# Kernel optimization log

Hardware: AMD Instinct MI355X
Metric: run time of the kernel (lower is better)

Reference implementation:

```python
import jax, jax.numpy as jnp
import numpy as np

UNITS = 512
LN_EPS = 1e-3  # Keras LayerNormalization default epsilon


def _lstm_cell(x, h, c, W, U, b):
    # Keras LSTMCell: z = x@W + h@U + b, gate order [i, f, g, o]
    z = x @ W + h @ U + b
    i, f, g, o = jnp.split(z, 4, axis=-1)
    i = jax.nn.sigmoid(i)
    f = jax.nn.sigmoid(f)
    g = jnp.tanh(g)
    o = jax.nn.sigmoid(o)
    c_new = f * c + i * g
    h_new = o * jnp.tanh(c_new)
    return h_new, c_new


def _layernorm(x, gamma, beta):
    mu = jnp.mean(x, axis=-1, keepdims=True)
    var = jnp.mean(jnp.square(x - mu), axis=-1, keepdims=True)
    return (x - mu) * jax.lax.rsqrt(var + LN_EPS) * gamma + beta


def setup_inputs() -> dict:
    key = jax.random.key(0)
    ks = jax.random.split(key, 8)
    B, T, F, U, C = 128, 1000, 72, UNITS, 14
    s = 0.05
    return {
        "x": jax.random.normal(ks[0], (B, T, F), jnp.float32),
        "w0": jax.random.normal(ks[1], (F, 4 * U), jnp.float32) * s,
        "u0": jax.random.normal(ks[2], (U, 4 * U), jnp.float32) * s,
        "b0": jnp.zeros((4 * U,), jnp.float32),
        "gamma": jnp.ones((U,), jnp.float32),
        "beta": jnp.zeros((U,), jnp.float32),
        "w1": jax.random.normal(ks[3], (U, 4 * U), jnp.float32) * s,
        "u1": jax.random.normal(ks[4], (U, 4 * U), jnp.float32) * s,
        "b1": jnp.zeros((4 * U,), jnp.float32),
        "wf": jax.random.normal(ks[5], (U, C), jnp.float32) * s,
        "bf": jnp.zeros((C,), jnp.float32),
    }


def reference(x, w0, u0, b0, gamma, beta, w1, u1, b1, wf, bf):
    B = x.shape[0]
    U = UNITS
    xt = jnp.transpose(x, (1, 0, 2))  # [T, B, F] time-major
    init = (
        jnp.zeros((B, U), x.dtype), jnp.zeros((B, U), x.dtype),  # h0, c0
        jnp.zeros((B, U), x.dtype), jnp.zeros((B, U), x.dtype),  # h1, c1
    )

    def step(carry, x_t):
        h0, c0, h1, c1 = carry
        h0, c0 = _lstm_cell(x_t, h0, c0, w0, u0, b0)
        h0n = _layernorm(h0, gamma, beta)
        h1, c1 = _lstm_cell(h0n, h1, c1, w1, u1, b1)
        # dropout is identity at inference (training=False)
        y_t = jax.nn.softmax(h1 @ wf + bf, axis=-1)
        return (h0, c0, h1, c1), y_t

    _, ys = jax.lax.scan(step, init, xt)  # ys: [T, B, C]
    return jnp.transpose(ys, (1, 0, 2))   # [B, T, C]
```

## Files before the change

kernel.cpp:

```cpp
#include <hip/hip_runtime.h>
#include <cstdint>
#include <cstddef>

#define T_STEPS 1000
#define NU 512
#define NC 14

typedef unsigned short ushort_t;
typedef unsigned int uint_t;
typedef __attribute__((ext_vector_type(8))) short bf16x8;
typedef __attribute__((ext_vector_type(4))) float f32x4;

#define OFF_BP0H  0u
#define OFF_BP0L  (OFF_BP0H + 128u*9728u*2u)
#define OFF_BP1H  (OFF_BP0L + 128u*9728u*2u)
#define OFF_BP1L  (OFF_BP1H + 128u*16384u*2u)
#define OFF_S1P   (OFF_BP1L + 128u*16384u*2u)
#define OFF_ZB1P  (OFF_S1P  + 2048u*4u)
#define OFF_B0P   (OFF_ZB1P + 2048u*4u)
#define OFF_WFT   (OFF_B0P  + 2048u*4u)
#define OFF_H0H   (OFF_WFT  + 14u*512u*4u)
#define OFF_H0L   (OFF_H0H  + 262144u)
#define OFF_H1H   (OFF_H0L  + 262144u)
#define OFF_H1L   (OFF_H1H  + 262144u)
#define OFF_CTR   (OFF_H1L  + 262144u)

#define SLOT_C0SUB  0
#define SLOT_C0ROOT (8*64)
#define SLOT_C1SUB  (16*64)
#define SLOT_C1ROOT (24*64)

__device__ __forceinline__ float bf2f(short s) {
    unsigned u = ((unsigned)(unsigned short)s) << 16;
    return __builtin_bit_cast(float, u);
}
__device__ __forceinline__ ushort_t f2bf(float f) {
    unsigned u = __float_as_uint(f);
    u = u + 0x7FFFu + ((u >> 16) & 1u);
    return (ushort_t)(u >> 16);
}

__global__ void pack0_kernel(const float* __restrict__ w0, const float* __restrict__ u0,
                             ushort_t* __restrict__ bp0h, ushort_t* __restrict__ bp0l)
{
    const int ntile = blockIdx.x;
    const int l = threadIdx.x & 63;
    const int c = l & 15, koff = (l >> 4) * 8;
    const int zcol = ntile * 4 + (c >> 2) + 512 * (c & 3);
    for (int s = (threadIdx.x >> 6); s < 19; s += 4) {
        bf16x8 hv, lv;
#pragma unroll
        for (int j = 0; j < 8; ++j) {
            int k = s * 32 + koff + j;
            float v;
            if (k < 96) v = (k < 72) ? w0[(size_t)k * 2048 + zcol] : 0.f;
            else        v = u0[(size_t)(k - 96) * 2048 + zcol];
            ushort_t hi = f2bf(v);
            ushort_t lo = f2bf(v - bf2f((short)hi));
            hv[j] = (short)hi; lv[j] = (short)lo;
        }
        size_t di = ((size_t)(ntile * 19 + s) * 64 + l) * 8;
        *(bf16x8*)&bp0h[di] = hv;
        *(bf16x8*)&bp0l[di] = lv;
    }
}

__global__ void pack1_kernel(const float* __restrict__ w1, const float* __restrict__ u1,
                             const float* __restrict__ gamma,
                             ushort_t* __restrict__ bp1h, ushort_t* __restrict__ bp1l)
{
    const int ntile = blockIdx.x;
    const int l = threadIdx.x & 63;
    const int c = l & 15, koff = (l >> 4) * 8;
    const int zcol = ntile * 4 + (c >> 2) + 512 * (c & 3);
    for (int s = (threadIdx.x >> 6); s < 32; s += 4) {
        bf16x8 hv, lv;
#pragma unroll
        for (int j = 0; j < 8; ++j) {
            int k = s * 32 + koff + j;
            float v = (k < 512) ? gamma[k] * w1[(size_t)k * 2048 + zcol]
                                : u1[(size_t)(k - 512) * 2048 + zcol];
            ushort_t hi = f2bf(v);
            ushort_t lo = f2bf(v - bf2f((short)hi));
            hv[j] = (short)hi; lv[j] = (short)lo;
        }
        size_t di = ((size_t)(ntile * 32 + s) * 64 + l) * 8;
        *(bf16x8*)&bp1h[di] = hv;
        *(bf16x8*)&bp1l[di] = lv;
    }
}

__global__ void sums_kernel(const float* __restrict__ w1, const float* __restrict__ gamma,
                            const float* __restrict__ beta, const float* __restrict__ b0,
                            const float* __restrict__ b1,
                            float* __restrict__ s1p, float* __restrict__ zb1p,
                            float* __restrict__ b0p)
{
    int zcol = blockIdx.x * 256 + threadIdx.x;
    float gs = 0.f, bs = 0.f;
    for (int k = 0; k < NU; k++) {
        float w = w1[(size_t)k * 2048 + zcol];
        gs += gamma[k] * w;
        bs += beta[k] * w;
    }
    int g = zcol >> 9, r = zcol & 511, nt = r >> 2, u = r & 3;
    int pc = nt * 16 + u * 4 + g;
    s1p[pc]  = gs;
    zb1p[pc] = b1[zcol] + bs;
    b0p[pc]  = b0[zcol];
}

__global__ void wft_kernel(const float* __restrict__ wf, float* __restrict__ wfT)
{
    int i = blockIdx.x * 512 + threadIdx.x;
    if (i < NC * NU) {
        int c = i >> 9, u = i & 511;
        wfT[c * NU + u] = wf[(size_t)u * NC + c];
    }
}

__global__ void init_kernel(char* __restrict__ ws)
{
    size_t i = (size_t)blockIdx.x * 1024 + threadIdx.x;
    uint_t* st = (uint_t*)(ws + OFF_H0H);
    if (i < 262144) st[i] = 0u;
    if (i < 2048) ((uint_t*)(ws + OFF_CTR))[i] = 0u;
}

__device__ __forceinline__ float sigf(float x)     { return 1.f / (1.f + __expf(-x)); }
__device__ __forceinline__ float tanhfast(float x) { return 2.f / (1.f + __expf(-2.f * x)) - 1.f; }

__device__ __forceinline__ void wait_ge(const unsigned* p, unsigned tgt)
{
    while (__hip_atomic_load(p, __ATOMIC_RELAXED, __HIP_MEMORY_SCOPE_AGENT) < tgt)
        __builtin_amdgcn_s_sleep(1);
}

__device__ __forceinline__ void publish(unsigned* sub, unsigned* root)
{
    unsigned old = __hip_atomic_fetch_add(sub, 1u, __ATOMIC_RELAXED, __HIP_MEMORY_SCOPE_AGENT);
    if ((old & 15u) == 15u)
        __hip_atomic_fetch_add(root, 16u, __ATOMIC_RELAXED, __HIP_MEMORY_SCOPE_AGENT);
}

__device__ void ypass(const ushort_t* __restrict__ h1h, const ushort_t* __restrict__ h1l,
                      const float* __restrict__ wfT, const float* __restrict__ bf,
                      float* __restrict__ out, int b, int tw, int lane)
{
    bf16x8 hh = *(const bf16x8*)(h1h + (size_t)b * NU + lane * 8);
    bf16x8 hl = *(const bf16x8*)(h1l + (size_t)b * NU + lane * 8);
    float hv[8];
#pragma unroll
    for (int j = 0; j < 8; ++j) hv[j] = bf2f(hh[j]) + bf2f(hl[j]);
    float z[NC];
#pragma unroll
    for (int c = 0; c < NC; ++c) {
        const float* wp = wfT + c * NU + lane * 8;
        float a = 0.f;
#pragma unroll
        for (int j = 0; j < 8; ++j) a = fmaf(hv[j], wp[j], a);
        z[c] = a;
    }
#pragma unroll
    for (int off = 32; off > 0; off >>= 1) {
#pragma unroll
        for (int c = 0; c < NC; ++c) z[c] += __shfl_xor(z[c], off);
    }
    if (lane == 0) {
        float mx = -1e30f;
#pragma unroll
        for (int c = 0; c < NC; ++c) { z[c] += bf[c]; mx = fmaxf(mx, z[c]); }
        float s = 0.f, e[NC];
#pragma unroll
        for (int c = 0; c < NC; ++c) { e[c] = __expf(z[c] - mx); s += e[c]; }
        float inv = 1.f / s;
        float* o = out + ((size_t)b * T_STEPS + tw) * NC;
#pragma unroll
        for (int c = 0; c < NC; ++c) o[c] = e[c] * inv;
    }
}

#define MFMA(A,B,C) __builtin_amdgcn_mfma_f32_16x16x32_bf16((A),(B),(C),0,0,0)

__global__ __launch_bounds__(512, 1)
void lstm_main(const float* __restrict__ x, const float* __restrict__ bf,
               char* __restrict__ ws, float* __restrict__ out)
{
    __shared__ __attribute__((aligned(16))) unsigned char smem[98304];

    const float* __restrict__ s1p  = (const float*)(ws + OFF_S1P);
    const float* __restrict__ zb1p = (const float*)(ws + OFF_ZB1P);
    const float* __restrict__ b0p  = (const float*)(ws + OFF_B0P);
    const float* __restrict__ wfT  = (const float*)(ws + OFF_WFT);
    ushort_t* h0h = (ushort_t*)(ws + OFF_H0H);
    ushort_t* h0l = (ushort_t*)(ws + OFF_H0L);
    ushort_t* h1h = (ushort_t*)(ws + OFF_H1H);
    ushort_t* h1l = (ushort_t*)(ws + OFF_H1L);
    unsigned* ctr = (unsigned*)(ws + OFF_CTR);

    const int tid  = threadIdx.x;
    const int l    = tid & 63;
    const int w    = tid >> 6;
    const int rr   = l & 15;
    const int koff = (l >> 4) * 8;
    const int blk  = blockIdx.x;
    const int erow = tid >> 2, eu = tid & 3;

    unsigned* C0root = ctr + SLOT_C0ROOT;
    unsigned* C1root = ctr + SLOT_C1ROOT;

    if (blk < 128) {
        const int ntile = blk;
        ushort_t* bpAh = (ushort_t*)smem;
        ushort_t* bpAl = (ushort_t*)(smem + 19456);
        ushort_t* xsh  = (ushort_t*)(smem + 38912);
        ushort_t* xsl  = (ushort_t*)(smem + 63488);
        float*    zex  = (float*)(smem + 88064);
        unsigned* C0sub = ctr + SLOT_C0SUB + (blk & 7) * 64;

        {
            const uint_t* sh = (const uint_t*)(ws + OFF_BP0H) + (size_t)ntile * 4864;
            const uint_t* sl = (const uint_t*)(ws + OFF_BP0L) + (size_t)ntile * 4864;
            uint_t* dh = (uint_t*)bpAh; uint_t* dl = (uint_t*)bpAl;
            for (int i = tid; i < 4864; i += 512) { dh[i] = sh[i]; dl[i] = sl[i]; }
            uint_t* xz = (uint_t*)xsh;
            for (int i = tid; i < 12288; i += 512) xz[i] = 0u;
        }
        const f32x4 b0v = *(const f32x4*)&b0p[ntile * 16 + eu * 4];
        float c0v = 0.f;
        const int m = w;
        const int rowA = m * 16 + rr;
        __syncthreads();

#pragma unroll 1
        for (int t = 0; t < T_STEPS; ++t) {
            const int cur = t & 1, prv = cur ^ 1;
            ushort_t* __restrict__       h0h_cur = h0h + cur * 65536;
            ushort_t* __restrict__       h0l_cur = h0l + cur * 65536;
            const ushort_t* __restrict__ h0h_prv = h0h + prv * 65536;
            const ushort_t* __restrict__ h0l_prv = h0l + prv * 65536;

#pragma unroll
            for (int i = 0; i < 18; ++i) {
                int e = tid + i * 512;
                int row = e / 72, k = e - row * 72;
                float v = x[(size_t)row * 72000 + (size_t)t * 72 + k];
                ushort_t hi = f2bf(v);
                ushort_t lo = f2bf(v - bf2f((short)hi));
                int di = (((row >> 4) * 3 + (k >> 5)) * 64 + ((k >> 3) & 3) * 16 + (row & 15)) * 8 + (k & 7);
                xsh[di] = hi; xsl[di] = lo;
            }
            if (tid == 0) {
                if (t >= 1) wait_ge(C0root, 128u * (unsigned)t);
                if (t >= 2) wait_ge(C1root, 128u * (unsigned)(t - 1));
                __threadfence();
            }
            __syncthreads();

            f32x4 aHH = {0,0,0,0}, aLH = {0,0,0,0}, aHL = {0,0,0,0};
#pragma unroll
            for (int s = 0; s < 3; ++s) {
                bf16x8 ah = *(const bf16x8*)&xsh[((m * 3 + s) * 64 + l) * 8];
                bf16x8 al = *(const bf16x8*)&xsl[((m * 3 + s) * 64 + l) * 8];
                bf16x8 bh = *(const bf16x8*)&bpAh[s * 512 + l * 8];
                bf16x8 bl = *(const bf16x8*)&bpAl[s * 512 + l * 8];
                aHH = MFMA(ah, bh, aHH); aLH = MFMA(al, bh, aLH); aHL = MFMA(ah, bl, aHL);
            }
            {
                const ushort_t* hph = h0h_prv + rowA * 512 + koff;
                const ushort_t* hpl = h0l_prv + rowA * 512 + koff;
#pragma unroll
                for (int s = 3; s < 19; ++s) {
                    bf16x8 ah = *(const bf16x8*)(hph + (s - 3) * 32);
                    bf16x8 al = *(const bf16x8*)(hpl + (s - 3) * 32);
                    bf16x8 bh = *(const bf16x8*)&bpAh[s * 512 + l * 8];
                    bf16x8 bl = *(const bf16x8*)&bpAl[s * 512 + l * 8];
                    aHH = MFMA(ah, bh, aHH); aLH = MFMA(al, bh, aLH); aHL = MFMA(ah, bl, aHL);
                }
            }
            f32x4 zv = aHH + aLH + aHL;
#pragma unroll
            for (int r = 0; r < 4; ++r)
                zex[(m * 16 + (l >> 4) * 4 + r) * 20 + rr] = zv[r];
            __syncthreads();

            {
                f32x4 z = *(const f32x4*)&zex[erow * 20 + eu * 4];
                z.x += b0v.x; z.y += b0v.y; z.z += b0v.z; z.w += b0v.w;
                float ig = sigf(z.x), fg = sigf(z.y), gg = tanhfast(z.z), og = sigf(z.w);
                float cn = fg * c0v + ig * gg;
                c0v = cn;
                float hval = og * tanhfast(cn);
                ushort_t hi = f2bf(hval);
                ushort_t lo = f2bf(hval - bf2f((short)hi));
                int idx = erow * 512 + ntile * 4 + eu;
                h0h_cur[idx] = hi; h0l_cur[idx] = lo;
            }
            __syncthreads();
            if (tid == 0) { __threadfence(); publish(C0sub, C0root); }
        }
    } else {
        const int ntile = blk - 128;
        ushort_t* bpBh = (ushort_t*)smem;
        ushort_t* bpBl = (ushort_t*)(smem + 32768);
        float* zexG = (float*)(smem + 65536);
        float* zexU = (float*)(smem + 75776);
        float* sqs  = (float*)(smem + 86016);
        float* sqq  = (float*)(smem + 86528);
        unsigned* C1sub = ctr + SLOT_C1SUB + (blk & 7) * 64;

        {
            const uint_t* sh = (const uint_t*)(ws + OFF_BP1H) + (size_t)ntile * 8192;
            const uint_t* sl = (const uint_t*)(ws + OFF_BP1L) + (size_t)ntile * 8192;
            uint_t* dh = (uint_t*)bpBh; uint_t* dl = (uint_t*)bpBl;
            for (int i = tid; i < 8192; i += 512) { dh[i] = sh[i]; dl[i] = sl[i]; }
        }
        const f32x4 s1v = *(const f32x4*)&s1p[ntile * 16 + eu * 4];
        const f32x4 zbv = *(const f32x4*)&zb1p[ntile * 16 + eu * 4];
        float c1v = 0.f;
        const int m = w;
        const int rowA = m * 16 + rr;
        __syncthreads();

#pragma unroll 1
        for (int t = 0; t < T_STEPS; ++t) {
            const int cur = t & 1, prv = cur ^ 1;
            const ushort_t* __restrict__ h0h_cur = h0h + cur * 65536;
            const ushort_t* __restrict__ h0l_cur = h0l + cur * 65536;
            ushort_t* __restrict__       h1h_cur = h1h + cur * 65536;
            ushort_t* __restrict__       h1l_cur = h1l + cur * 65536;
            const ushort_t* __restrict__ h1h_prv = h1h + prv * 65536;
            const ushort_t* __restrict__ h1l_prv = h1l + prv * 65536;

            if (tid == 0) {
                if (t >= 1) wait_ge(C1root, 128u * (unsigned)t);
                __threadfence();
            }
            __syncthreads();

            f32x4 uHH = {0,0,0,0}, uLH = {0,0,0,0}, uHL = {0,0,0,0};
            {
                const ushort_t* hph = h1h_prv + rowA * 512 + koff;
                const ushort_t* hpl = h1l_prv + rowA * 512 + koff;
#pragma unroll
                for (int s = 0; s < 16; ++s) {
                    bf16x8 ah = *(const bf16x8*)(hph + s * 32);
                    bf16x8 al = *(const bf16x8*)(hpl + s * 32);
                    bf16x8 bh = *(const bf16x8*)&bpBh[(16 + s) * 512 + l * 8];
                    bf16x8 bl = *(const bf16x8*)&bpBl[(16 + s) * 512 + l * 8];
                    uHH = MFMA(ah, bh, uHH); uLH = MFMA(al, bh, uLH); uHL = MFMA(ah, bl, uHL);
                }
            }
            if (w == 7 && t > 0) ypass(h1h_prv, h1l_prv, wfT, bf, out, ntile, t - 1, l);

            if (tid == 0) {
                wait_ge(C0root, 128u * (unsigned)(t + 1));
                __threadfence();
            }
            __syncthreads();

            f32x4 gHH = {0,0,0,0}, gLH = {0,0,0,0}, gHL = {0,0,0,0};
            float sa = 0.f, qa = 0.f;
            {
                const ushort_t* hph = h0h_cur + rowA * 512 + koff;
                const ushort_t* hpl = h0l_cur + rowA * 512 + koff;
#pragma unroll
                for (int s = 0; s < 16; ++s) {
                    bf16x8 ah = *(const bf16x8*)(hph + s * 32);
                    bf16x8 al = *(const bf16x8*)(hpl + s * 32);
                    bf16x8 bh = *(const bf16x8*)&bpBh[s * 512 + l * 8];
                    bf16x8 bl = *(const bf16x8*)&bpBl[s * 512 + l * 8];
                    gHH = MFMA(ah, bh, gHH); gLH = MFMA(al, bh, gLH); gHL = MFMA(ah, bl, gHL);
#pragma unroll
                    for (int j = 0; j < 8; ++j) {
                        float hv = bf2f(ah[j]) + bf2f(al[j]);
                        sa += hv; qa = fmaf(hv, hv, qa);
                    }
                }
            }
            sa += __shfl_xor(sa, 16); sa += __shfl_xor(sa, 32);
            qa += __shfl_xor(qa, 16); qa += __shfl_xor(qa, 32);
            if (l < 16) { sqs[m * 16 + l] = sa; sqq[m * 16 + l] = qa; }
            f32x4 zG = gHH + gLH + gHL, zU = uHH + uLH + uHL;
#pragma unroll
            for (int r = 0; r < 4; ++r) {
                zexG[(m * 16 + (l >> 4) * 4 + r) * 20 + rr] = zG[r];
                zexU[(m * 16 + (l >> 4) * 4 + r) * 20 + rr] = zU[r];
            }
            __syncthreads();

            {
                float mu = sqs[erow] * (1.f / 512.f);
                float rs = rsqrtf(sqq[erow] * (1.f / 512.f) - mu * mu + 1e-3f);
                f32x4 zg = *(const f32x4*)&zexG[erow * 20 + eu * 4];
                f32x4 zu = *(const f32x4*)&zexU[erow * 20 + eu * 4];
                float z0 = rs * (zg.x - mu * s1v.x) + zu.x + zbv.x;
                float z1 = rs * (zg.y - mu * s1v.y) + zu.y + zbv.y;
                float z2 = rs * (zg.z - mu * s1v.z) + zu.z + zbv.z;
                float z3 = rs * (zg.w - mu * s1v.w) + zu.w + zbv.w;
                float ig = sigf(z0), fg = sigf(z1), gg = tanhfast(z2), og = sigf(z3);
                float cn = fg * c1v + ig * gg;
                c1v = cn;
                float hval = og * tanhfast(cn);
                ushort_t hi = f2bf(hval);
                ushort_t lo = f2bf(hval - bf2f((short)hi));
                int idx = erow * 512 + ntile * 4 + eu;
                h1h_cur[idx] = hi; h1l_cur[idx] = lo;
            }
            __syncthreads();
            if (tid == 0) { __threadfence(); publish(C1sub, C1root); }
        }

        if (tid == 0) { wait_ge(C1root, 128u * (unsigned)T_STEPS); __threadfence(); }
        __syncthreads();
        if (w == 7)
            ypass(h1h + ((T_STEPS - 1) & 1) * 65536, h1l + ((T_STEPS - 1) & 1) * 65536,
                  wfT, bf, out, ntile, T_STEPS - 1, l);
    }
}

extern "C" void kernel_launch(void* const* d_in, const int* in_sizes, int n_in,
                              void* d_out, int out_size, void* d_ws, size_t ws_size,
                              hipStream_t stream)
{
    const float* x     = (const float*)d_in[0];
    const float* w0    = (const float*)d_in[1];
    const float* u0    = (const float*)d_in[2];
    const float* b0    = (const float*)d_in[3];
    const float* gamma = (const float*)d_in[4];
    const float* beta  = (const float*)d_in[5];
    const float* w1    = (const float*)d_in[6];
    const float* u1    = (const float*)d_in[7];
    const float* b1    = (const float*)d_in[8];
    const float* wf    = (const float*)d_in[9];
    const float* bf    = (const float*)d_in[10];
    float* out = (float*)d_out;
    char* ws   = (char*)d_ws;

    hipLaunchKernelGGL(pack0_kernel, dim3(128), dim3(256), 0, stream,
                       w0, u0, (ushort_t*)(ws + OFF_BP0H), (ushort_t*)(ws + OFF_BP0L));
    hipLaunchKernelGGL(pack1_kernel, dim3(128), dim3(256), 0, stream,
                       w1, u1, gamma, (ushort_t*)(ws + OFF_BP1H), (ushort_t*)(ws + OFF_BP1L));
    hipLaunchKernelGGL(sums_kernel, dim3(8), dim3(256), 0, stream,
                       w1, gamma, beta, b0, b1,
                       (float*)(ws + OFF_S1P), (float*)(ws + OFF_ZB1P), (float*)(ws + OFF_B0P));
    hipLaunchKernelGGL(wft_kernel, dim3(14), dim3(512), 0, stream, wf, (float*)(ws + OFF_WFT));
    hipLaunchKernelGGL(init_kernel, dim3(256), dim3(1024), 0, stream, ws);

    const float* xp  = x;
    const float* bfp = bf;
    char*  wsp  = ws;
    float* outp = out;
    void* args[] = { (void*)&xp, (void*)&bfp, (void*)&wsp, (void*)&outp };
    hipLaunchCooperativeKernel((void*)lstm_main, dim3(256), dim3(512), args, 0, stream);
}
```

Before: 35.32 ms.

## Replace hierarchical atomic counters with per-block flags polled wave-wide, prefetch x, cache wf

Each block now publishes its progress by storing the step number into its own flag slot, replacing the two-level fetch_add counter tree. Wave 0 waits by polling all 128 flags per layer in parallel and leaves when every flag has reached the target. The layer-0 wait is moved after the input-projection MFMAs so it can overlap that work, and the next step's x values are prefetched into registers during the current step. The output-projection weights are copied into LDS for the layer-1 blocks. The aim is to cut atomic contention and serial wait latency on the per-step barrier, at the cost of more polling traffic and more registers and LDS.

```diff
diff --git a/kernel.cpp b/kernel.cpp
--- a/kernel.cpp
+++ b/kernel.cpp
@@ -23,12 +23,8 @@
 #define OFF_H0L   (OFF_H0H  + 262144u)
 #define OFF_H1H   (OFF_H0L  + 262144u)
 #define OFF_H1L   (OFF_H1H  + 262144u)
-#define OFF_CTR   (OFF_H1L  + 262144u)
-
-#define SLOT_C0SUB  0
-#define SLOT_C0ROOT (8*64)
-#define SLOT_C1SUB  (16*64)
-#define SLOT_C1ROOT (24*64)
+#define OFF_FLG0  (OFF_H1L  + 262144u)
+#define OFF_FLG1  (OFF_FLG0 + 512u)
 
 __device__ __forceinline__ float bf2f(short s) {
     unsigned u = ((unsigned)(unsigned short)s) << 16;
@@ -124,23 +120,37 @@
     size_t i = (size_t)blockIdx.x * 1024 + threadIdx.x;
     uint_t* st = (uint_t*)(ws + OFF_H0H);
     if (i < 262144) st[i] = 0u;
-    if (i < 2048) ((uint_t*)(ws + OFF_CTR))[i] = 0u;
+    if (i < 256) ((uint_t*)(ws + OFF_FLG0))[i] = 0u;
 }
 
 __device__ __forceinline__ float sigf(float x)     { return 1.f / (1.f + __expf(-x)); }
 __device__ __forceinline__ float tanhfast(float x) { return 2.f / (1.f + __expf(-2.f * x)) - 1.f; }
 
-__device__ __forceinline__ void wait_ge(const unsigned* p, unsigned tgt)
-{
-    while (__hip_atomic_load(p, __ATOMIC_RELAXED, __HIP_MEMORY_SCOPE_AGENT) < tgt)
-        __builtin_amdgcn_s_sleep(1);
-}
-
-__device__ __forceinline__ void publish(unsigned* sub, unsigned* root)
-{
-    unsigned old = __hip_atomic_fetch_add(sub, 1u, __ATOMIC_RELAXED, __HIP_MEMORY_SCOPE_AGENT);
-    if ((old & 15u) == 15u)
-        __hip_atomic_fetch_add(root, 16u, __ATOMIC_RELAXED, __HIP_MEMORY_SCOPE_AGENT);
+__device__ __forceinline__ void wave_wait(const unsigned* f, unsigned tgt, int l)
+{
+    while (true) {
+        unsigned a = __hip_atomic_load(f + l,      __ATOMIC_RELAXED, __HIP_MEMORY_SCOPE_AGENT);
+        unsigned b = __hip_atomic_load(f + 64 + l, __ATOMIC_RELAXED, __HIP_MEMORY_SCOPE_AGENT);
+        if (__all((a >= tgt) && (b >= tgt))) return;
+        __builtin_amdgcn_s_sleep(2);
+    }
+}
+__device__ __forceinline__ void wave_wait2(const unsigned* f0, unsigned t0,
+                                           const unsigned* f1, unsigned t1, int l)
+{
+    while (true) {
+        unsigned a0 = __hip_atomic_load(f0 + l,      __ATOMIC_RELAXED, __HIP_MEMORY_SCOPE_AGENT);
+        unsigned b0 = __hip_atomic_load(f0 + 64 + l, __ATOMIC_RELAXED, __HIP_MEMORY_SCOPE_AGENT);
+        unsigned a1 = __hip_atomic_load(f1 + l,      __ATOMIC_RELAXED, __HIP_MEMORY_SCOPE_AGENT);
+        unsigned b1 = __hip_atomic_load(f1 + 64 + l, __ATOMIC_RELAXED, __HIP_MEMORY_SCOPE_AGENT);
+        if (__all((a0 >= t0) && (b0 >= t0) && (a1 >= t1) && (b1 >= t1))) return;
+        __builtin_amdgcn_s_sleep(2);
+    }
+}
+__device__ __forceinline__ void publish_flag(unsigned* f, int idx, unsigned val)
+{
+    __threadfence();
+    __hip_atomic_store(f + idx, val, __ATOMIC_RELAXED, __HIP_MEMORY_SCOPE_AGENT);
 }
 
 __device__ void ypass(const ushort_t* __restrict__ h1h, const ushort_t* __restrict__ h1l,
@@ -186,17 +196,18 @@
 void lstm_main(const float* __restrict__ x, const float* __restrict__ bf,
                char* __restrict__ ws, float* __restrict__ out)
 {
-    __shared__ __attribute__((aligned(16))) unsigned char smem[98304];
+    __shared__ __attribute__((aligned(16))) unsigned char smem[115712];
 
     const float* __restrict__ s1p  = (const float*)(ws + OFF_S1P);
     const float* __restrict__ zb1p = (const float*)(ws + OFF_ZB1P);
     const float* __restrict__ b0p  = (const float*)(ws + OFF_B0P);
-    const float* __restrict__ wfT  = (const float*)(ws + OFF_WFT);
+    const float* __restrict__ wfTg = (const float*)(ws + OFF_WFT);
     ushort_t* h0h = (ushort_t*)(ws + OFF_H0H);
     ushort_t* h0l = (ushort_t*)(ws + OFF_H0L);
     ushort_t* h1h = (ushort_t*)(ws + OFF_H1H);
     ushort_t* h1l = (ushort_t*)(ws + OFF_H1L);
-    unsigned* ctr = (unsigned*)(ws + OFF_CTR);
+    unsigned* flag0 = (unsigned*)(ws + OFF_FLG0);
+    unsigned* flag1 = (unsigned*)(ws + OFF_FLG1);
 
     const int tid  = threadIdx.x;
     const int l    = tid & 63;
@@ -206,9 +217,6 @@
     const int blk  = blockIdx.x;
     const int erow = tid >> 2, eu = tid & 3;
 
-    unsigned* C0root = ctr + SLOT_C0ROOT;
-    unsigned* C1root = ctr + SLOT_C1ROOT;
-
     if (blk < 128) {
         const int ntile = blk;
         ushort_t* bpAh = (ushort_t*)smem;
@@ -216,7 +224,6 @@
         ushort_t* xsh  = (ushort_t*)(smem + 38912);
         ushort_t* xsl  = (ushort_t*)(smem + 63488);
         float*    zex  = (float*)(smem + 88064);
-        unsigned* C0sub = ctr + SLOT_C0SUB + (blk & 7) * 64;
 
         {
             const uint_t* sh = (const uint_t*)(ws + OFF_BP0H) + (size_t)ntile * 4864;
@@ -230,6 +237,13 @@
         float c0v = 0.f;
         const int m = w;
         const int rowA = m * 16 + rr;
+
+        float xr[18];
+#pragma unroll
+        for (int i = 0; i < 18; ++i) {
+            int e = tid + i * 512, row = e / 72, k = e - row * 72;
+            xr[i] = x[(size_t)row * 72000 + k];
+        }
         __syncthreads();
 
 #pragma unroll 1
@@ -242,18 +256,12 @@
 
 #pragma unroll
             for (int i = 0; i < 18; ++i) {
-                int e = tid + i * 512;
-                int row = e / 72, k = e - row * 72;
-                float v = x[(size_t)row * 72000 + (size_t)t * 72 + k];
+                int e = tid + i * 512, row = e / 72, k = e - row * 72;
+                float v = xr[i];
                 ushort_t hi = f2bf(v);
                 ushort_t lo = f2bf(v - bf2f((short)hi));
                 int di = (((row >> 4) * 3 + (k >> 5)) * 64 + ((k >> 3) & 3) * 16 + (row & 15)) * 8 + (k & 7);
                 xsh[di] = hi; xsl[di] = lo;
-            }
-            if (tid == 0) {
-                if (t >= 1) wait_ge(C0root, 128u * (unsigned)t);
-                if (t >= 2) wait_ge(C1root, 128u * (unsigned)(t - 1));
-                __threadfence();
             }
             __syncthreads();
 
@@ -266,6 +274,19 @@
                 bf16x8 bl = *(const bf16x8*)&bpAl[s * 512 + l * 8];
                 aHH = MFMA(ah, bh, aHH); aLH = MFMA(al, bh, aLH); aHL = MFMA(ah, bl, aHL);
             }
+            if (t + 1 < T_STEPS) {
+#pragma unroll
+                for (int i = 0; i < 18; ++i) {
+                    int e = tid + i * 512, row = e / 72, k = e - row * 72;
+                    xr[i] = x[(size_t)row * 72000 + (size_t)(t + 1) * 72 + k];
+                }
+            }
+            if (w == 0 && t >= 1) {
+                wave_wait2(flag0, (unsigned)t, flag1, (t >= 2) ? (unsigned)(t - 1) : 0u, l);
+                __threadfence();
+            }
+            __syncthreads();
+
             {
                 const ushort_t* hph = h0h_prv + rowA * 512 + koff;
                 const ushort_t* hpl = h0l_prv + rowA * 512 + koff;
@@ -297,23 +318,24 @@
                 h0h_cur[idx] = hi; h0l_cur[idx] = lo;
             }
             __syncthreads();
-            if (tid == 0) { __threadfence(); publish(C0sub, C0root); }
+            if (tid == 0) publish_flag(flag0, blk, (unsigned)(t + 1));
         }
     } else {
         const int ntile = blk - 128;
         ushort_t* bpBh = (ushort_t*)smem;
         ushort_t* bpBl = (ushort_t*)(smem + 32768);
-        float* zexG = (float*)(smem + 65536);
-        float* zexU = (float*)(smem + 75776);
-        float* sqs  = (float*)(smem + 86016);
-        float* sqq  = (float*)(smem + 86528);
-        unsigned* C1sub = ctr + SLOT_C1SUB + (blk & 7) * 64;
+        float* wfTl = (float*)(smem + 65536);
+        float* zexG = (float*)(smem + 94208);
+        float* zexU = (float*)(smem + 104448);
+        float* sqs  = (float*)(smem + 114688);
+        float* sqq  = (float*)(smem + 115200);
 
         {
             const uint_t* sh = (const uint_t*)(ws + OFF_BP1H) + (size_t)ntile * 8192;
             const uint_t* sl = (const uint_t*)(ws + OFF_BP1L) + (size_t)ntile * 8192;
             uint_t* dh = (uint_t*)bpBh; uint_t* dl = (uint_t*)bpBl;
             for (int i = tid; i < 8192; i += 512) { dh[i] = sh[i]; dl[i] = sl[i]; }
+            for (int i = tid; i < 7168; i += 512) wfTl[i] = wfTg[i];
         }
         const f32x4 s1v = *(const f32x4*)&s1p[ntile * 16 + eu * 4];
         const f32x4 zbv = *(const f32x4*)&zb1p[ntile * 16 + eu * 4];
@@ -332,8 +354,8 @@
             const ushort_t* __restrict__ h1h_prv = h1h + prv * 65536;
             const ushort_t* __restrict__ h1l_prv = h1l + prv * 65536;
 
-            if (tid == 0) {
-                if (t >= 1) wait_ge(C1root, 128u * (unsigned)t);
+            if (w == 0 && t >= 1) {
+                wave_wait(flag1, (unsigned)t, l);
                 __threadfence();
             }
             __syncthreads();
@@ -351,10 +373,10 @@
                     uHH = MFMA(ah, bh, uHH); uLH = MFMA(al, bh, uLH); uHL = MFMA(ah, bl, uHL);
                 }
             }
-            if (w == 7 && t > 0) ypass(h1h_prv, h1l_prv, wfT, bf, out, ntile, t - 1, l);
-
-            if (tid == 0) {
-                wait_ge(C0root, 128u * (unsigned)(t + 1));
+            if (w == 7 && t > 0) ypass(h1h_prv, h1l_prv, wfTl, bf, out, ntile, t - 1, l);
+
+            if (w == 0) {
+                wave_wait(flag0, (unsigned)(t + 1), l);
                 __threadfence();
             }
             __syncthreads();
@@ -408,14 +430,14 @@
                 h1h_cur[idx] = hi; h1l_cur[idx] = lo;
             }
             __syncthreads();
-            if (tid == 0) { __threadfence(); publish(C1sub, C1root); }
-        }
-
-        if (tid == 0) { wait_ge(C1root, 128u * (unsigned)T_STEPS); __threadfence(); }
+            if (tid == 0) publish_flag(flag1, ntile, (unsigned)(t + 1));
+        }
+
+        if (w == 0) { wave_wait(flag1, (unsigned)T_STEPS, l); __threadfence(); }
         __syncthreads();
         if (w == 7)
             ypass(h1h + ((T_STEPS - 1) & 1) * 65536, h1l + ((T_STEPS - 1) & 1) * 65536,
-                  wfT, bf, out, ntile, T_STEPS - 1, l);
+                  wfTl, bf, out, ntile, T_STEPS - 1, l);
     }
 }
 
```

Result: faster. 33.43 ms (-5.4%).
